# Kernel optimization log

Measured on AMD Instinct MI355X. Metric: run time of the kernel, lower is better.

Reference implementation:

```python
import jax, jax.numpy as jnp
import numpy as np

NUM_AA, EMB, H = 20, 16, 128
IN1 = 1 + 2 + 4 * EMB  # 67: theta, sin/cos phi, 4-residue context
IN2 = 2 + 2 + 4 * EMB  # 68: sin/cos phi_i, sin/cos phi_{i+1}, context


def setup_inputs() -> dict:
    key = jax.random.key(0)
    ks = jax.random.split(key, 12)
    B, L = 64, 4096
    R = jax.random.normal(ks[0], (B, L, 3), dtype=jnp.float32)
    seq = jax.random.randint(ks[1], (B, L), 0, NUM_AA)
    def lin(k, i, o):
        kw, kb = jax.random.split(k)
        s = 1.0 / np.sqrt(i)
        return (jax.random.uniform(kw, (i, o), jnp.float32, -s, s),
                jax.random.uniform(kb, (o,), jnp.float32, -s, s))
    emb = jax.random.normal(ks[2], (NUM_AA, EMB), dtype=jnp.float32)
    tp_W1, tp_b1 = lin(ks[3], IN1, H)
    tp_W2, tp_b2 = lin(ks[4], H, H)
    tp_W3, tp_b3 = lin(ks[5], H, 1)
    pp_W1, pp_b1 = lin(ks[6], IN2, H)
    pp_W2, pp_b2 = lin(ks[7], H, H)
    pp_W3, pp_b3 = lin(ks[8], H, 1)
    return dict(R=R, seq=seq, emb=emb,
                tp_W1=tp_W1, tp_b1=tp_b1, tp_W2=tp_W2, tp_b2=tp_b2, tp_W3=tp_W3, tp_b3=tp_b3,
                pp_W1=pp_W1, pp_b1=pp_b1, pp_W2=pp_W2, pp_b2=pp_b2, pp_W3=pp_W3, pp_b3=pp_b3)


def _mlp(x, W1, b1, W2, b2, W3, b3):
    h = jax.nn.relu(x @ W1 + b1)
    h = jax.nn.relu(h @ W2 + b2)
    return x @ 0.0 if False else h @ W3 + b3


def _bond_angles(R):
    # angle at residue i+1 of triplet (i, i+1, i+2) -> (B, L-2)
    u1 = R[:, :-2] - R[:, 1:-1]
    u2 = R[:, 2:] - R[:, 1:-1]
    c = jnp.cross(u1, u2)
    return jnp.arctan2(jnp.linalg.norm(c, axis=-1), jnp.sum(u1 * u2, axis=-1))


def _torsions(R):
    # dihedral of quadruplet (i..i+3) -> (B, L-3)
    b1 = R[:, 1:-2] - R[:, :-3]
    b2 = R[:, 2:-1] - R[:, 1:-2]
    b3 = R[:, 3:] - R[:, 2:-1]
    n1 = jnp.cross(b1, b2)
    n2 = jnp.cross(b2, b3)
    b2n = b2 / (jnp.linalg.norm(b2, axis=-1, keepdims=True) + 1e-8)
    x = jnp.sum(n1 * n2, axis=-1)
    y = jnp.sum(jnp.cross(n1, n2) * b2n, axis=-1)
    return jnp.arctan2(y, x)


def reference(R, seq, emb,
              tp_W1, tp_b1, tp_W2, tp_b2, tp_W3, tp_b3,
              pp_W1, pp_b1, pp_W2, pp_b2, pp_W3, pp_b3):
    B, L, _ = R.shape
    e = emb[seq]                                   # (B, L, EMB)
    theta = _bond_angles(R)                        # (B, L-2)
    phi = _torsions(R)                             # (B, L-3)
    sc_phi = jnp.stack([jnp.sin(phi), jnp.cos(phi)], axis=-1)  # (B, L-3, 2)
    theta_in = jnp.cos(theta[:, :L - 3])           # use_cos_theta=True
    ctx = jnp.concatenate([e[:, :-3], e[:, 1:-2], e[:, 2:-1], e[:, 3:]], axis=-1)  # (B, L-3, 4*EMB)
    x1 = jnp.concatenate([theta_in[..., None], sc_phi, ctx], axis=-1)  # (B, L-3, 67)
    E1 = _mlp(x1, tp_W1, tp_b1, tp_W2, tp_b2, tp_W3, tp_b3)[..., 0].sum(axis=1)
    x2 = jnp.concatenate([sc_phi[:, :-1], sc_phi[:, 1:], ctx[:, :-1]], axis=-1)    # (B, L-4, 68)
    E2 = _mlp(x2, pp_W1, pp_b1, pp_W2, pp_b2, pp_W3, pp_b3)[..., 0].sum(axis=1)
    return E1 + E2
```

## Files before the change

kernel.cpp:

```cpp
#include <hip/hip_runtime.h>

#define L_   4096
#define LIM0 4093
#define LIM1 4092

typedef short s16x8 __attribute__((ext_vector_type(8)));
typedef float f32x4 __attribute__((ext_vector_type(4)));

__device__ __forceinline__ unsigned short f2bf(float f) {
    union { float f; unsigned int u; } v; v.f = f;
    unsigned int r = v.u + 0x7FFFu + ((v.u >> 16) & 1u);
    return (unsigned short)(r >> 16);
}

__device__ __forceinline__ unsigned int cvt_pk_bf16(float lo, float hi) {
    unsigned int r;
    asm("v_cvt_pk_bf16_f32 %0, %1, %2" : "=v"(r) : "v"(lo), "v"(hi));
    return r;
}

struct F3 { float x, y, z; };
__device__ __forceinline__ F3 ld3(const float* p) { return F3{p[0], p[1], p[2]}; }
__device__ __forceinline__ F3 sub3(F3 a, F3 b) { return F3{a.x-b.x, a.y-b.y, a.z-b.z}; }
__device__ __forceinline__ F3 cross3(F3 a, F3 b) {
    return F3{a.y*b.z - a.z*b.y, a.z*b.x - a.x*b.z, a.x*b.y - a.y*b.x};
}
__device__ __forceinline__ float dot3(F3 a, F3 b) { return a.x*b.x + a.y*b.y + a.z*b.z; }

__device__ __forceinline__ void torsion(F3 a, F3 b, F3 c, F3 d, float& sn, float& cs) {
    F3 v1 = sub3(b, a), v2 = sub3(c, b), v3 = sub3(d, c);
    F3 n1 = cross3(v1, v2), n2 = cross3(v2, v3);
    float x = dot3(n1, n2);
    F3 m = cross3(n1, n2);
    float bn = sqrtf(dot3(v2, v2)) + 1e-8f;
    float y = dot3(m, v2) / bn;
    float inv = rsqrtf(x*x + y*y + 1e-30f);
    sn = y * inv; cs = x * inv;
}

__device__ __forceinline__ void xstore(unsigned short* S, int rr, int c, unsigned short v) {
    S[rr*128 + (((c >> 3) ^ (rr & 7)) << 3) + (c & 7)] = v;
}

__global__ __launch_bounds__(256) void ss_feat(const float* __restrict__ R,
                                               uint2* __restrict__ feat) {
    const int p = blockIdx.x * 256 + threadIdx.x;
    const int b = blockIdx.y;
    if (p >= LIM0) return;
    const float* Rp = R + ((size_t)(b * L_ + p)) * 3;
    F3 p0 = ld3(Rp), p1 = ld3(Rp + 3), p2 = ld3(Rp + 6), p3 = ld3(Rp + 9);
    F3 u1 = sub3(p0, p1), u2 = sub3(p2, p1);
    F3 cr = cross3(u1, u2);
    float d = dot3(u1, u2);
    float ct = d * rsqrtf(d * d + dot3(cr, cr) + 1e-30f);
    float sp, cp; torsion(p0, p1, p2, p3, sp, cp);
    feat[(size_t)b * L_ + p] = make_uint2(cvt_pk_bf16(ct, 1.0f), cvt_pk_bf16(sp, cp));
}

__global__ __launch_bounds__(256) void ss_mlp(
    const int* __restrict__ seq, const uint2* __restrict__ feat, const float* __restrict__ emb,
    const float* __restrict__ tpW1, const float* __restrict__ tpb1,
    const float* __restrict__ tpW2, const float* __restrict__ tpb2,
    const float* __restrict__ ppW1, const float* __restrict__ ppb1,
    const float* __restrict__ ppW2, const float* __restrict__ ppb2,
    float* __restrict__ ws) {

    __shared__ __align__(16) unsigned short Xs[64*128];
    __shared__ __align__(16) unsigned short H1s[64*128];
    __shared__ uint4 embs4[40];

    const int b = blockIdx.y, mode = blockIdx.z;
    const int lim  = mode ? LIM1 : LIM0;
    const float* W1  = mode ? ppW1 : tpW1;
    const float* Bi1 = mode ? ppb1 : tpb1;
    const float* W2  = mode ? ppW2 : tpW2;
    const float* Bi2 = mode ? ppb2 : tpb2;

    const int t = threadIdx.x;
    const int w = t >> 6, l = t & 63, g = l >> 4, ln = l & 15;
    const int lw = ln & 7;
    const int r = t >> 2, sub = t & 3;
    const int rw = r & 7;

    int aa_; uint2 fv_, fv2_;
    {
        const int posc = min(blockIdx.x * 64 + r, lim - 1);
        aa_ = seq[b * L_ + posc + sub];
        if (sub == 0) {
            fv_ = feat[(size_t)b * L_ + posc];
            if (mode) fv2_ = feat[(size_t)b * L_ + posc + 1];
        }
    }

    if (t < 40) {
        const float* ep = emb + (t >> 1) * 16 + (t & 1) * 8;
        embs4[t] = make_uint4(cvt_pk_bf16(ep[0], ep[1]), cvt_pk_bf16(ep[2], ep[3]),
                              cvt_pk_bf16(ep[4], ep[5]), cvt_pk_bf16(ep[6], ep[7]));
    }
    for (int i = t; i < 1024; i += 256) ((uint4*)Xs)[i] = make_uint4(0u, 0u, 0u, 0u);

    s16x8 a1f[2][3]; s16x8 a2f[2][4];
    float bb2[2][4];
    #pragma unroll
    for (int mt = 0; mt < 2; mt++) {
        const int hc = w*32 + mt*16 + ln;
        #pragma unroll
        for (int kk = 0; kk < 3; kk++)
            #pragma unroll
            for (int j = 0; j < 8; j++) {
                const int c = kk*32 + g*8 + j;
                int kp;
                if (mode) kp = (c < 64) ? c + 4 : ((c < 68) ? c - 64 : ((c == 68) ? -2 : -1));
                else      kp = (c < 64) ? c + 3 : ((c == 64) ? 0 : ((c == 65) ? -2 :
                               ((c == 66) ? 1 : ((c == 67) ? 2 : -1))));
                float wv = (kp == -1) ? 0.f : ((kp == -2) ? Bi1[hc] : W1[kp*128 + hc]);
                a1f[mt][kk][j] = (short)f2bf(wv);
            }
        #pragma unroll
        for (int kk = 0; kk < 4; kk++)
            #pragma unroll
            for (int j = 0; j < 8; j++)
                a2f[mt][kk][j] = (short)f2bf(W2[(kk*32 + g*8 + j)*128 + hc]);
        #pragma unroll
        for (int i = 0; i < 4; i++) bb2[mt][i] = Bi2[w*32 + mt*16 + g*4 + i];
    }

    __syncthreads();

    {
        uint4 e0 = embs4[aa_*2], e1 = embs4[aa_*2 + 1];
        *(uint4*)(Xs + r*128 + (((sub*2    ) ^ rw) << 3)) = e0;
        *(uint4*)(Xs + r*128 + (((sub*2 + 1) ^ rw) << 3)) = e1;
        if (sub == 0) {
            uint2 u = mode ? make_uint2(fv_.y, fv2_.y) : fv_;
            *(uint2*)(Xs + r*128 + ((8 ^ rw) << 3)) = u;
        }
    }
    if (t < 64) xstore(Xs, t, 68, (unsigned short)0x3F80);
    __syncthreads();

    float s[2][4] = {{0.f,0.f,0.f,0.f},{0.f,0.f,0.f,0.f}};

    for (int tile = blockIdx.x; tile < 64; tile += 8) {
        const int pos0 = tile << 6;
        const bool has_next = (tile + 8) < 64;

        if (has_next) {
            const int posc = min(pos0 + 512 + r, lim - 1);
            aa_ = seq[b * L_ + posc + sub];
            if (sub == 0) {
                fv_ = feat[(size_t)b * L_ + posc];
                if (mode) fv2_ = feat[(size_t)b * L_ + posc + 1];
            }
        }

        #pragma unroll
        for (int pt = 0; pt < 4; pt++) {
            const int row = pt*16 + ln;
            const unsigned short* base = Xs + row*128;
            f32x4 c0 = {0.f,0.f,0.f,0.f}, c1 = {0.f,0.f,0.f,0.f};
            #pragma unroll
            for (int kk = 0; kk < 3; kk++) {
                s16x8 bf = *(const s16x8*)(base + (((kk*4 + g) ^ lw) << 3));
                c0 = __builtin_amdgcn_mfma_f32_16x16x32_bf16(a1f[0][kk], bf, c0, 0, 0, 0);
                c1 = __builtin_amdgcn_mfma_f32_16x16x32_bf16(a1f[1][kk], bf, c1, 0, 0, 0);
            }
            unsigned short* hb = H1s + row*128;
            {
                uint2 u;
                u.x = cvt_pk_bf16(fmaxf(c0[0], 0.f), fmaxf(c0[1], 0.f));
                u.y = cvt_pk_bf16(fmaxf(c0[2], 0.f), fmaxf(c0[3], 0.f));
                *(uint2*)(hb + ((((w*4) + (g>>1)) ^ lw) << 3) + (g&1)*4) = u;
            }
            {
                uint2 u;
                u.x = cvt_pk_bf16(fmaxf(c1[0], 0.f), fmaxf(c1[1], 0.f));
                u.y = cvt_pk_bf16(fmaxf(c1[2], 0.f), fmaxf(c1[3], 0.f));
                *(uint2*)(hb + ((((w*4 + 2) + (g>>1)) ^ lw) << 3) + (g&1)*4) = u;
            }
        }
        __syncthreads();

        if (has_next) {
            uint4 e0 = embs4[aa_*2], e1 = embs4[aa_*2 + 1];
            *(uint4*)(Xs + r*128 + (((sub*2    ) ^ rw) << 3)) = e0;
            *(uint4*)(Xs + r*128 + (((sub*2 + 1) ^ rw) << 3)) = e1;
            if (sub == 0) {
                uint2 u = mode ? make_uint2(fv_.y, fv2_.y) : fv_;
                *(uint2*)(Xs + r*128 + ((8 ^ rw) << 3)) = u;
            }
        }

        #pragma unroll
        for (int pt = 0; pt < 4; pt++) {
            const int row = pt*16 + ln;
            const unsigned short* base = H1s + row*128;
            f32x4 d0 = {0.f,0.f,0.f,0.f}, d1 = {0.f,0.f,0.f,0.f};
            #pragma unroll
            for (int kk = 0; kk < 4; kk++) {
                s16x8 bf = *(const s16x8*)(base + (((kk*4 + g) ^ lw) << 3));
                d0 = __builtin_amdgcn_mfma_f32_16x16x32_bf16(a2f[0][kk], bf, d0, 0, 0, 0);
                d1 = __builtin_amdgcn_mfma_f32_16x16x32_bf16(a2f[1][kk], bf, d1, 0, 0, 0);
            }
            if (pos0 + row < lim) {
                #pragma unroll
                for (int i = 0; i < 4; i++) {
                    s[0][i] += fmaxf(d0[i] + bb2[0][i], 0.f);
                    s[1][i] += fmaxf(d1[i] + bb2[1][i], 0.f);
                }
            }
        }
        __syncthreads();
    }

    #pragma unroll
    for (int mt = 0; mt < 2; mt++)
        #pragma unroll
        for (int i = 0; i < 4; i++) {
            float v = s[mt][i];
            v += __shfl_xor(v, 1, 64); v += __shfl_xor(v, 2, 64);
            v += __shfl_xor(v, 4, 64); v += __shfl_xor(v, 8, 64);
            if (ln == 0)
                atomicAdd(ws + ((b*2 + mode) << 7) + w*32 + mt*16 + g*4 + i, v);
        }
}

__global__ void ss_finish(const float* __restrict__ ws,
                          const float* __restrict__ tpW3, const float* __restrict__ tpb3,
                          const float* __restrict__ ppW3, const float* __restrict__ ppb3,
                          float* __restrict__ out) {
    const int b = blockIdx.x, t = threadIdx.x;
    float v = ws[(b*2 + 0)*128 + t] * tpW3[t] + ws[(b*2 + 1)*128 + t] * ppW3[t];
    #pragma unroll
    for (int off = 1; off < 64; off <<= 1) v += __shfl_xor(v, off, 64);
    __shared__ float ps[2];
    if ((t & 63) == 0) ps[t >> 6] = v;
    __syncthreads();
    if (t == 0) out[b] = ps[0] + ps[1] + 4093.f * tpb3[0] + 4092.f * ppb3[0];
}

extern "C" void kernel_launch(void* const* d_in, const int* in_sizes, int n_in,
                              void* d_out, int out_size, void* d_ws, size_t ws_size,
                              hipStream_t stream) {
    (void)in_sizes; (void)n_in; (void)out_size; (void)ws_size;
    const float* R    = (const float*)d_in[0];
    const int*   seq  = (const int*)d_in[1];
    const float* emb  = (const float*)d_in[2];
    const float* tpW1 = (const float*)d_in[3];
    const float* tpb1 = (const float*)d_in[4];
    const float* tpW2 = (const float*)d_in[5];
    const float* tpb2 = (const float*)d_in[6];
    const float* tpW3 = (const float*)d_in[7];
    const float* tpb3 = (const float*)d_in[8];
    const float* ppW1 = (const float*)d_in[9];
    const float* ppb1 = (const float*)d_in[10];
    const float* ppW2 = (const float*)d_in[11];
    const float* ppb2 = (const float*)d_in[12];
    const float* ppW3 = (const float*)d_in[13];
    const float* ppb3 = (const float*)d_in[14];
    float* ws   = (float*)d_ws;
    uint2* feat = (uint2*)((char*)d_ws + 65536);

    hipMemsetAsync(ws, 0, 64*2*128*sizeof(float), stream);
    ss_feat<<<dim3(16, 64), 256, 0, stream>>>(R, feat);
    ss_mlp<<<dim3(8, 64, 2), 256, 0, stream>>>(seq, feat, emb,
                                               tpW1, tpb1, tpW2, tpb2,
                                               ppW1, ppb1, ppW2, ppb2, ws);
    ss_finish<<<64, 128, 0, stream>>>(ws, tpW3, tpb3, ppW3, ppb3, (float*)d_out);
}
```

Baseline: 51.18 us.

## Precompute bf16 embedding table globally and deepen input prefetch to two tiles

```diff
diff --git a/kernel.cpp b/kernel.cpp
--- a/kernel.cpp
+++ b/kernel.cpp
@@ -43,7 +43,14 @@
 }
 
 __global__ __launch_bounds__(256) void ss_feat(const float* __restrict__ R,
-                                               uint2* __restrict__ feat) {
+                                               uint2* __restrict__ feat,
+                                               const float* __restrict__ emb,
+                                               uint4* __restrict__ embbf) {
+    if (blockIdx.x == 0 && blockIdx.y == 0 && threadIdx.x < 40) {
+        const float* ep = emb + (threadIdx.x >> 1) * 16 + (threadIdx.x & 1) * 8;
+        embbf[threadIdx.x] = make_uint4(cvt_pk_bf16(ep[0], ep[1]), cvt_pk_bf16(ep[2], ep[3]),
+                                        cvt_pk_bf16(ep[4], ep[5]), cvt_pk_bf16(ep[6], ep[7]));
+    }
     const int p = blockIdx.x * 256 + threadIdx.x;
     const int b = blockIdx.y;
     if (p >= LIM0) return;
@@ -58,7 +65,8 @@
 }
 
 __global__ __launch_bounds__(256) void ss_mlp(
-    const int* __restrict__ seq, const uint2* __restrict__ feat, const float* __restrict__ emb,
+    const int* __restrict__ seq, const uint2* __restrict__ feat,
+    const uint4* __restrict__ embbf,
     const float* __restrict__ tpW1, const float* __restrict__ tpb1,
     const float* __restrict__ tpW2, const float* __restrict__ tpb2,
     const float* __restrict__ ppW1, const float* __restrict__ ppb1,
@@ -67,9 +75,8 @@
 
     __shared__ __align__(16) unsigned short Xs[64*128];
     __shared__ __align__(16) unsigned short H1s[64*128];
-    __shared__ uint4 embs4[40];
-
-    const int b = blockIdx.y, mode = blockIdx.z;
+
+    const int b = blockIdx.y, mode = blockIdx.z, bx = blockIdx.x;
     const int lim  = mode ? LIM1 : LIM0;
     const float* W1  = mode ? ppW1 : tpW1;
     const float* Bi1 = mode ? ppb1 : tpb1;
@@ -81,22 +88,21 @@
     const int lw = ln & 7;
     const int r = t >> 2, sub = t & 3;
     const int rw = r & 7;
-
-    int aa_; uint2 fv_, fv2_;
+    const size_t bL = (size_t)b * L_;
+
+    int aa0, aa_nxt; uint2 fv0 = {}, fv0b = {}, fvn = {}, fvnb = {};
     {
-        const int posc = min(blockIdx.x * 64 + r, lim - 1);
-        aa_ = seq[b * L_ + posc + sub];
+        const int p0 = min(bx * 64 + r, lim - 1);
+        aa0 = seq[bL + p0 + sub];
+        const int p1 = min(bx * 64 + 512 + r, lim - 1);
+        aa_nxt = seq[bL + p1 + sub];
         if (sub == 0) {
-            fv_ = feat[(size_t)b * L_ + posc];
-            if (mode) fv2_ = feat[(size_t)b * L_ + posc + 1];
-        }
-    }
-
-    if (t < 40) {
-        const float* ep = emb + (t >> 1) * 16 + (t & 1) * 8;
-        embs4[t] = make_uint4(cvt_pk_bf16(ep[0], ep[1]), cvt_pk_bf16(ep[2], ep[3]),
-                              cvt_pk_bf16(ep[4], ep[5]), cvt_pk_bf16(ep[6], ep[7]));
-    }
+            fv0 = feat[bL + p0];
+            fvn = feat[bL + p1];
+            if (mode) { fv0b = feat[bL + p0 + 1]; fvnb = feat[bL + p1 + 1]; }
+        }
+    }
+
     for (int i = t; i < 1024; i += 256) ((uint4*)Xs)[i] = make_uint4(0u, 0u, 0u, 0u);
 
     s16x8 a1f[2][3]; s16x8 a2f[2][4];
@@ -125,14 +131,15 @@
         for (int i = 0; i < 4; i++) bb2[mt][i] = Bi2[w*32 + mt*16 + g*4 + i];
     }
 
+    uint4 e0_ = embbf[aa0*2], e1_ = embbf[aa0*2 + 1];
+
     __syncthreads();
 
     {
-        uint4 e0 = embs4[aa_*2], e1 = embs4[aa_*2 + 1];
-        *(uint4*)(Xs + r*128 + (((sub*2    ) ^ rw) << 3)) = e0;
-        *(uint4*)(Xs + r*128 + (((sub*2 + 1) ^ rw) << 3)) = e1;
+        *(uint4*)(Xs + r*128 + (((sub*2    ) ^ rw) << 3)) = e0_;
+        *(uint4*)(Xs + r*128 + (((sub*2 + 1) ^ rw) << 3)) = e1_;
         if (sub == 0) {
-            uint2 u = mode ? make_uint2(fv_.y, fv2_.y) : fv_;
+            uint2 u = mode ? make_uint2(fv0.y, fv0b.y) : fv0;
             *(uint2*)(Xs + r*128 + ((8 ^ rw) << 3)) = u;
         }
     }
@@ -141,16 +148,18 @@
 
     float s[2][4] = {{0.f,0.f,0.f,0.f},{0.f,0.f,0.f,0.f}};
 
-    for (int tile = blockIdx.x; tile < 64; tile += 8) {
-        const int pos0 = tile << 6;
-        const bool has_next = (tile + 8) < 64;
-
-        if (has_next) {
-            const int posc = min(pos0 + 512 + r, lim - 1);
-            aa_ = seq[b * L_ + posc + sub];
+    for (int it = 0; it < 8; it++) {
+        const int pos0 = (bx + it*8) << 6;
+
+        uint4 e0n, e1n;
+        if (it < 7) { e0n = embbf[aa_nxt*2]; e1n = embbf[aa_nxt*2 + 1]; }
+        int aa2; uint2 fv2 = {}, fv2b = {};
+        if (it < 6) {
+            const int p2 = min((bx + (it+2)*8)*64 + r, lim - 1);
+            aa2 = seq[bL + p2 + sub];
             if (sub == 0) {
-                fv_ = feat[(size_t)b * L_ + posc];
-                if (mode) fv2_ = feat[(size_t)b * L_ + posc + 1];
+                fv2 = feat[bL + p2];
+                if (mode) fv2b = feat[bL + p2 + 1];
             }
         }
 
@@ -181,12 +190,11 @@
         }
         __syncthreads();
 
-        if (has_next) {
-            uint4 e0 = embs4[aa_*2], e1 = embs4[aa_*2 + 1];
-            *(uint4*)(Xs + r*128 + (((sub*2    ) ^ rw) << 3)) = e0;
-            *(uint4*)(Xs + r*128 + (((sub*2 + 1) ^ rw) << 3)) = e1;
+        if (it < 7) {
+            *(uint4*)(Xs + r*128 + (((sub*2    ) ^ rw) << 3)) = e0n;
+            *(uint4*)(Xs + r*128 + (((sub*2 + 1) ^ rw) << 3)) = e1n;
             if (sub == 0) {
-                uint2 u = mode ? make_uint2(fv_.y, fv2_.y) : fv_;
+                uint2 u = mode ? make_uint2(fvn.y, fvnb.y) : fvn;
                 *(uint2*)(Xs + r*128 + ((8 ^ rw) << 3)) = u;
             }
         }
@@ -211,6 +219,8 @@
             }
         }
         __syncthreads();
+
+        if (it < 6) { aa_nxt = aa2; fvn = fv2; fvnb = fv2b; }
     }
 
     #pragma unroll
@@ -258,12 +268,13 @@
     const float* ppb2 = (const float*)d_in[12];
     const float* ppW3 = (const float*)d_in[13];
     const float* ppb3 = (const float*)d_in[14];
-    float* ws   = (float*)d_ws;
-    uint2* feat = (uint2*)((char*)d_ws + 65536);
+    float* ws    = (float*)d_ws;
+    uint2* feat  = (uint2*)((char*)d_ws + 65536);
+    uint4* embbf = (uint4*)((char*)d_ws + 65536 + 2097152);
 
     hipMemsetAsync(ws, 0, 64*2*128*sizeof(float), stream);
-    ss_feat<<<dim3(16, 64), 256, 0, stream>>>(R, feat);
-    ss_mlp<<<dim3(8, 64, 2), 256, 0, stream>>>(seq, feat, emb,
+    ss_feat<<<dim3(16, 64), 256, 0, stream>>>(R, feat, emb, embbf);
+    ss_mlp<<<dim3(8, 64, 2), 256, 0, stream>>>(seq, feat, embbf,
                                                tpW1, tpb1, tpW2, tpb2,
                                                ppW1, ppb1, ppW2, ppb2, ws);
     ss_finish<<<64, 128, 0, stream>>>(ws, tpW3, tpb3, ppW3, ppb3, (float*)d_out);
```

New measurement: 54.78 us. +7.0%, slower.
